# Optimization experiments

Hardware: AMD Instinct MI355X
Metric: run time of the kernel (lower is better)

The kernel has to match this reference:

```python
import jax, jax.numpy as jnp
import numpy as np

D = 1024
H = 16
DK = D // H
HID = 4096
EPS = 1e-5


def setup_inputs() -> dict:
    key = jax.random.key(0)
    ks = jax.random.split(key, 16)
    B, S = 2, 2048
    sc = lambda fan_in: 1.0 / np.sqrt(fan_in)
    inp = {
        "x": jax.random.normal(ks[0], (B, S, D), jnp.float32),
        "y": jax.random.normal(ks[1], (B, S, D), jnp.float32),
        "mask": jnp.ones((B, 1, 1, S), jnp.int32),
        # attention projections, stored [in, out]
        "Wq": jax.random.normal(ks[2], (D, D), jnp.float32) * sc(D),
        "bq": jnp.zeros((D,), jnp.float32),
        "Wk": jax.random.normal(ks[3], (D, D), jnp.float32) * sc(D),
        "bk": jnp.zeros((D,), jnp.float32),
        "Wv": jax.random.normal(ks[4], (D, D), jnp.float32) * sc(D),
        "bv": jnp.zeros((D,), jnp.float32),
        "Wo": jax.random.normal(ks[5], (D, D), jnp.float32) * sc(D),
        "bo": jnp.zeros((D,), jnp.float32),
        # FFN
        "W1": jax.random.normal(ks[6], (D, HID), jnp.float32) * sc(D),
        "b1": jnp.zeros((HID,), jnp.float32),
        "W2": jax.random.normal(ks[7], (HID, D), jnp.float32) * sc(HID),
        "b2": jnp.zeros((D,), jnp.float32),
        # LayerNorms
        "g1": jnp.ones((D,), jnp.float32),
        "be1": jnp.zeros((D,), jnp.float32),
        "g2": jnp.ones((D,), jnp.float32),
        "be2": jnp.zeros((D,), jnp.float32),
    }
    return inp


def _layer_norm(x, g, b):
    m = jnp.mean(x, axis=-1, keepdims=True)
    v = jnp.mean(jnp.square(x - m), axis=-1, keepdims=True)
    return (x - m) * jax.lax.rsqrt(v + EPS) * g + b


def _split_heads(t):  # [B,S,D] -> [B,H,S,DK]
    B, S, _ = t.shape
    return t.reshape(B, S, H, DK).transpose(0, 2, 1, 3)


def reference(x, y, mask, Wq, bq, Wk, bk, Wv, bv, Wo, bo,
              W1, b1, W2, b2, g1, be1, g2, be2):
    scale = 1.0 / np.sqrt(DK)
    Q = _split_heads(x @ Wq + bq)
    K = _split_heads(y @ Wk + bk)
    V = _split_heads(y @ Wv + bv)
    scores = jnp.einsum("bhqd,bhkd->bhqk", Q, K) * scale  # [B,H,S,S]
    scores = jnp.where(mask == 0, jnp.float32(-1e9), scores)
    probs = jax.nn.softmax(scores, axis=-1)
    attn = jnp.einsum("bhqk,bhkd->bhqd", probs, V)
    B, _, S, _ = attn.shape
    attn = attn.transpose(0, 2, 1, 3).reshape(B, S, D)
    mha_out = attn @ Wo + bo
    x1 = _layer_norm(x + mha_out, g1, be1)
    ff = jax.nn.relu(x1 @ W1 + b1) @ W2 + b2
    return _layer_norm(x1 + ff, g2, be2)
```

## Files before the change

### kernel.cpp

```cpp
#include <hip/hip_runtime.h>

#define S_ 2048
#define D_ 1024
#define B_ 2
#define H_ 16
#define DK_ 64
#define HID_ 4096

typedef unsigned short u16;
typedef __attribute__((ext_vector_type(8))) short short8;
typedef __attribute__((ext_vector_type(4))) float f32x4;

#define SLOT(q16, r16) (((q16) * 16) + ((r16) ^ (q16)))

__device__ __forceinline__ float bf2f(u16 u) {
  return __uint_as_float(((unsigned int)u) << 16);
}
__device__ __forceinline__ u16 f2bf(float f) {
  unsigned int x = __float_as_uint(f);
  x += 0x7fff + ((x >> 16) & 1);
  return (u16)(x >> 16);
}
__device__ __forceinline__ unsigned int pk2bf(float lo, float hi) {
  return ((__float_as_uint(lo) + 0x8000u) >> 16) | ((__float_as_uint(hi) + 0x8000u) & 0xffff0000u);
}

__global__ void prep_k(
    const float* __restrict__ Wq, const float* __restrict__ Wk,
    const float* __restrict__ Wv, const float* __restrict__ Wo,
    const float* __restrict__ W1, const float* __restrict__ W2,
    u16* __restrict__ WqT, u16* __restrict__ WkT, u16* __restrict__ WvT,
    u16* __restrict__ WoT, u16* __restrict__ W1T, u16* __restrict__ W2T) {
  const int z = blockIdx.z;
  __shared__ u16 tile[32][33];
  const float* in; u16* outp; int R, C;
  switch (z) {
    case 0: in = Wq; outp = WqT; R = 1024; C = 1024; break;
    case 1: in = Wk; outp = WkT; R = 1024; C = 1024; break;
    case 2: in = Wv; outp = WvT; R = 1024; C = 1024; break;
    case 3: in = Wo; outp = WoT; R = 1024; C = 1024; break;
    case 4: in = W1; outp = W1T; R = 1024; C = 4096; break;
    default: in = W2; outp = W2T; R = 4096; C = 1024; break;
  }
  int c0, r0;
  if (z == 5) { c0 = blockIdx.y * 32; r0 = blockIdx.x * 32; }
  else        { c0 = blockIdx.x * 32; r0 = blockIdx.y * 32; }
  if (c0 >= C || r0 >= R) return;
  const int tx = threadIdx.x, ty = threadIdx.y;
  for (int i = ty; i < 32; i += 8)
    tile[i][tx] = f2bf(in[(long)(r0 + i) * C + c0 + tx]);
  __syncthreads();
  for (int i = ty; i < 32; i += 8)
    outp[(long)(c0 + i) * R + r0 + tx] = tile[tx][i];
}

__global__ __launch_bounds__(256) void cvt2_k(const float* __restrict__ x, const float* __restrict__ y,
                                              u16* __restrict__ xb, u16* __restrict__ yb) {
  const int z = blockIdx.y;
  const float* in = z ? y : x;
  u16* outp = z ? yb : xb;
  const int i = blockIdx.x * 256 + threadIdx.x;
  float4 v = ((const float4*)in)[i];
  unsigned int lo = (unsigned int)f2bf(v.x) | ((unsigned int)f2bf(v.y) << 16);
  unsigned int hi = (unsigned int)f2bf(v.z) | ((unsigned int)f2bf(v.w) << 16);
  ((uint2*)outp)[i] = make_uint2(lo, hi);
}

template<int MT, int NT, int OUTF32>
__global__ __launch_bounds__(256) void gemm_bt(
    const u16* __restrict__ A, const u16* __restrict__ Bt,
    const float* __restrict__ bias, void* __restrict__ Cv,
    int K, int lda, int ldb, int ldc,
    long sA, long sB, long sC, int relu) {
  constexpr int BM = MT * 32;
  constexpr int BN = NT * 32;
  __shared__ __align__(16) u16 As[BM * 32];
  __shared__ __align__(16) u16 Bs[BN * 32];
  const int z = blockIdx.z;
  A  += (long)z * sA;
  Bt += (long)z * sB;
  const int tid  = threadIdx.x;
  const int lane = tid & 63, wave = tid >> 6;
  const int quad = lane >> 4, l15 = lane & 15;
  const int wm = wave >> 1, wn = wave & 1;
  const u16* Ab = A  + (long)(blockIdx.y * BM) * lda;
  const u16* Bb = Bt + (long)(blockIdx.x * BN) * ldb;

  f32x4 acc[MT][NT];
#pragma unroll
  for (int i = 0; i < MT; ++i)
#pragma unroll
    for (int j = 0; j < NT; ++j) acc[i][j] = (f32x4){0.f, 0.f, 0.f, 0.f};

  const int r0  = tid >> 2;
  const int kk0 = (tid & 3) * 8;

  for (int kt = 0; kt < K; kt += 32) {
#pragma unroll
    for (int p = 0; p < BM / 64; ++p) {
      __builtin_amdgcn_global_load_lds(
          (const __attribute__((address_space(1))) void*)(Ab + (long)(p * 64 + r0) * lda + kt + kk0),
          (__attribute__((address_space(3))) void*)(&As[p * 2048 + tid * 8]), 16, 0, 0);
    }
#pragma unroll
    for (int p = 0; p < BN / 64; ++p) {
      __builtin_amdgcn_global_load_lds(
          (const __attribute__((address_space(1))) void*)(Bb + (long)(p * 64 + r0) * ldb + kt + kk0),
          (__attribute__((address_space(3))) void*)(&Bs[p * 2048 + tid * 8]), 16, 0, 0);
    }
    __syncthreads();
    short8 af[MT], bfr[NT];
#pragma unroll
    for (int mt = 0; mt < MT; ++mt)
      af[mt] = *(const short8*)&As[(wm * (MT * 16) + mt * 16 + l15) * 32 + quad * 8];
#pragma unroll
    for (int nt = 0; nt < NT; ++nt)
      bfr[nt] = *(const short8*)&Bs[(wn * (NT * 16) + nt * 16 + l15) * 32 + quad * 8];
#pragma unroll
    for (int mt = 0; mt < MT; ++mt)
#pragma unroll
      for (int nt = 0; nt < NT; ++nt)
        acc[mt][nt] = __builtin_amdgcn_mfma_f32_16x16x32_bf16(af[mt], bfr[nt], acc[mt][nt], 0, 0, 0);
    __syncthreads();
  }

#pragma unroll
  for (int nt = 0; nt < NT; ++nt) {
    const int col = blockIdx.x * BN + wn * (NT * 16) + nt * 16 + l15;
    const float bvv = bias ? bias[col] : 0.f;
#pragma unroll
    for (int mt = 0; mt < MT; ++mt) {
#pragma unroll
      for (int r = 0; r < 4; ++r) {
        const int row = blockIdx.y * BM + wm * (MT * 16) + mt * 16 + quad * 4 + r;
        float v = acc[mt][nt][r] + bvv;
        if (relu) v = fmaxf(v, 0.f);
        if (OUTF32) ((float*)Cv)[(long)z * sC + (long)row * ldc + col] = v;
        else        ((u16*)Cv)[(long)z * sC + (long)row * ldc + col] = f2bf(v);
      }
    }
  }
}

template<int RELU>
__global__ __launch_bounds__(512, 2) void gemm256_k(
    const u16* __restrict__ A, const u16* __restrict__ Bt,
    const float* __restrict__ bias, u16* __restrict__ C,
    int K, int lda, int ldb, int ldc, int kOff, long sC) {
  __shared__ __align__(16) u16 lds[65536];
  const int z = blockIdx.z;
  A  += (long)z * kOff;
  Bt += (long)z * kOff;
  const int tid = threadIdx.x;
  const int lane = tid & 63, w = tid >> 6;
  const int quad = lane >> 4, l15 = lane & 15;
  const int wm = w >> 2, wn = w & 3;
  const int bx = blockIdx.x, by = blockIdx.y;

  const int srow = w * 16 + l15;
  const u16* a0p = A + (long)(by * 256 + srow) * lda + quad * 8;
  const u16* a1p = a0p + (long)128 * lda;
  const u16* b0p = Bt + (long)(bx * 256 + srow) * ldb + quad * 8;
  const u16* b1p = b0p + (long)128 * ldb;

  f32x4 acc[8][4];
#pragma unroll
  for (int i = 0; i < 8; ++i)
#pragma unroll
    for (int j = 0; j < 4; ++j) acc[i][j] = (f32x4){0.f, 0.f, 0.f, 0.f};

  auto STAGE = [&](int c) {
    const int sl = (c & 3) * 8192;
    const long ko = (long)c * 32;
    __builtin_amdgcn_global_load_lds(
        (const __attribute__((address_space(1))) void*)(a0p + ko),
        (__attribute__((address_space(3))) void*)(&lds[sl + tid * 8]), 16, 0, 0);
    __builtin_amdgcn_global_load_lds(
        (const __attribute__((address_space(1))) void*)(a1p + ko),
        (__attribute__((address_space(3))) void*)(&lds[sl + 4096 + tid * 8]), 16, 0, 0);
    __builtin_amdgcn_global_load_lds(
        (const __attribute__((address_space(1))) void*)(b0p + ko),
        (__attribute__((address_space(3))) void*)(&lds[32768 + sl + tid * 8]), 16, 0, 0);
    __builtin_amdgcn_global_load_lds(
        (const __attribute__((address_space(1))) void*)(b1p + ko),
        (__attribute__((address_space(3))) void*)(&lds[32768 + sl + 4096 + tid * 8]), 16, 0, 0);
  };

  auto COMPUTE = [&](int t) {
    const int sl = (t & 3) * 8192;
    short8 af[8], bfv[4];
#pragma unroll
    for (int fr = 0; fr < 8; ++fr)
      af[fr] = *(const short8*)&lds[sl + ((wm * 8 + fr) * 64 + lane) * 8];
#pragma unroll
    for (int fc = 0; fc < 4; ++fc)
      bfv[fc] = *(const short8*)&lds[32768 + sl + ((wn * 4 + fc) * 64 + lane) * 8];
    __builtin_amdgcn_s_setprio(1);
#pragma unroll
    for (int fr = 0; fr < 8; ++fr)
#pragma unroll
      for (int fc = 0; fc < 4; ++fc)
        acc[fr][fc] = __builtin_amdgcn_mfma_f32_16x16x32_bf16(af[fr], bfv[fc], acc[fr][fc], 0, 0, 0);
    __builtin_amdgcn_s_setprio(0);
  };

  const int NT = K >> 5;
  STAGE(0); STAGE(1); STAGE(2);
  for (int t = 0; t < NT - 2; ++t) {
    asm volatile("s_waitcnt vmcnt(8)" ::: "memory");
    __builtin_amdgcn_s_barrier();
    __builtin_amdgcn_sched_barrier(0);
    if (t + 3 < NT) STAGE(t + 3);
    COMPUTE(t);
  }
  asm volatile("s_waitcnt vmcnt(4)" ::: "memory");
  __builtin_amdgcn_s_barrier();
  __builtin_amdgcn_sched_barrier(0);
  COMPUTE(NT - 2);
  asm volatile("s_waitcnt vmcnt(0)" ::: "memory");
  __builtin_amdgcn_s_barrier();
  __builtin_amdgcn_sched_barrier(0);
  COMPUTE(NT - 1);

  C += (long)z * sC;
#pragma unroll
  for (int fc = 0; fc < 4; ++fc) {
    const int col = bx * 256 + wn * 64 + fc * 16 + l15;
    const float bvv = bias ? bias[col] : 0.f;
#pragma unroll
    for (int fr = 0; fr < 8; ++fr) {
      const long row = by * 256 + wm * 128 + fr * 16 + quad * 4;
#pragma unroll
      for (int r = 0; r < 4; ++r) {
        float v = acc[fr][fc][r] + bvv;
        if (RELU) v = fmaxf(v, 0.f);
        C[(row + r) * ldc + col] = f2bf(v);
      }
    }
  }
}

__global__ __launch_bounds__(256) void qkv_k(
    const u16* __restrict__ xb, const u16* __restrict__ yb,
    const u16* __restrict__ WqT, const u16* __restrict__ WkT, const u16* __restrict__ WvT,
    const float* __restrict__ bq, const float* __restrict__ bk, const float* __restrict__ bv,
    u16* __restrict__ Q, u16* __restrict__ Kp, u16* __restrict__ Vp) {
  __shared__ __align__(16) u16 As[128 * 32];
  __shared__ __align__(16) u16 Bs[128 * 32];
  const int z = blockIdx.z;
  const u16* A  = (z == 0) ? xb : yb;
  const u16* Bt = (z == 0) ? WqT : (z == 1) ? WkT : WvT;
  const float* bias = (z == 0) ? bq : (z == 1) ? bk : bv;
  u16* C = (z == 0) ? Q : (z == 1) ? Kp : Vp;
  const float sc = (z == 0) ? 0.18033688011112042f : 1.0f;
  const int tid  = threadIdx.x;
  const int lane = tid & 63, wave = tid >> 6;
  const int quad = lane >> 4, l15 = lane & 15;
  const int wm = wave >> 1, wn = wave & 1;
  const u16* Ab = A  + (long)(blockIdx.y * 128) * D_;
  const u16* Bb = Bt + (long)(blockIdx.x * 128) * D_;

  f32x4 acc[4][4];
#pragma unroll
  for (int i = 0; i < 4; ++i)
#pragma unroll
    for (int j = 0; j < 4; ++j) acc[i][j] = (f32x4){0.f, 0.f, 0.f, 0.f};

  const int r0  = tid >> 2;
  const int kk0 = (tid & 3) * 8;

  for (int kt = 0; kt < D_; kt += 32) {
#pragma unroll
    for (int p = 0; p < 2; ++p) {
      __builtin_amdgcn_global_load_lds(
          (const __attribute__((address_space(1))) void*)(Ab + (long)(p * 64 + r0) * D_ + kt + kk0),
          (__attribute__((address_space(3))) void*)(&As[p * 2048 + tid * 8]), 16, 0, 0);
      __builtin_amdgcn_global_load_lds(
          (const __attribute__((address_space(1))) void*)(Bb + (long)(p * 64 + r0) * D_ + kt + kk0),
          (__attribute__((address_space(3))) void*)(&Bs[p * 2048 + tid * 8]), 16, 0, 0);
    }
    __syncthreads();
    short8 af[4], bfr[4];
#pragma unroll
    for (int mt = 0; mt < 4; ++mt)
      af[mt] = *(const short8*)&As[(wm * 64 + mt * 16 + l15) * 32 + quad * 8];
#pragma unroll
    for (int nt = 0; nt < 4; ++nt)
      bfr[nt] = *(const short8*)&Bs[(wn * 64 + nt * 16 + l15) * 32 + quad * 8];
#pragma unroll
    for (int mt = 0; mt < 4; ++mt)
#pragma unroll
      for (int nt = 0; nt < 4; ++nt)
        acc[mt][nt] = __builtin_amdgcn_mfma_f32_16x16x32_bf16(af[mt], bfr[nt], acc[mt][nt], 0, 0, 0);
    __syncthreads();
  }

#pragma unroll
  for (int nt = 0; nt < 4; ++nt) {
    const int col = blockIdx.x * 128 + wn * 64 + nt * 16 + l15;
    const float bvv = bias[col];
#pragma unroll
    for (int mt = 0; mt < 4; ++mt) {
#pragma unroll
      for (int r = 0; r < 4; ++r) {
        const int row = blockIdx.y * 128 + wm * 64 + mt * 16 + quad * 4 + r;
        C[(long)row * D_ + col] = f2bf((acc[mt][nt][r] + bvv) * sc);
      }
    }
  }
}

__global__ void vtrans_k(const u16* __restrict__ V, u16* __restrict__ Vt) {
  __shared__ u16 tile[32][33];
  const int bh = blockIdx.z, b = bh >> 4, h = bh & 15;
  const u16* in = V + (long)b * S_ * D_ + h * DK_;
  u16* outp = Vt + (long)bh * DK_ * S_;
  const int s0 = blockIdx.x * 32, d0 = blockIdx.y * 32;
  const int tx = threadIdx.x, ty = threadIdx.y;
  for (int i = ty; i < 32; i += 8)
    tile[i][tx] = in[(long)(s0 + i) * D_ + d0 + tx];
  __syncthreads();
  for (int i = ty; i < 32; i += 8)
    outp[(long)(d0 + i) * S_ + s0 + tx] = tile[tx][i];
}

__global__ __launch_bounds__(256, 4) void flash_k(
    const u16* __restrict__ Q, const u16* __restrict__ Kp, const u16* __restrict__ Vt,
    const int* __restrict__ mask, u16* __restrict__ ctx) {
  __shared__ __align__(16) u16 sQ[8192];
  __shared__ __align__(16) u16 sK[2][2048];
  __shared__ __align__(16) u16 sV[2][2048];
  __shared__ __align__(16) u16 sP[4][1024];

  const int bh = blockIdx.x, qt = blockIdx.y;
  const int b = bh >> 4, h = bh & 15;
  const int tid = threadIdx.x;
  const int w = tid >> 6, lane = tid & 63;
  const int quad = lane >> 4, l15 = lane & 15;

  const u16* Qg  = Q  + ((long)b * S_ + qt * 128) * D_ + h * DK_;
  const u16* Kg  = Kp + (long)b * S_ * D_ + h * DK_;
  const u16* Vtg = Vt + (long)bh * DK_ * S_;
  const int* maskg = mask + (long)b * S_;
  u16* ctxg = ctx + ((long)b * S_ + qt * 128) * D_ + h * DK_;

  const int krow = tid >> 3, kc = tid & 7;
  const u16* kptr = Kg + (long)krow * D_ + kc * 8;
  const int ksw = (((krow >> 4) * 2 + (kc >> 2)) * 64 + SLOT(kc & 3, krow & 15)) * 8;
  const int vrow = tid >> 2, vc = tid & 3;
  const u16* vptr = Vtg + (long)vrow * S_ + vc * 8;
  const int vsw = ((vrow >> 4) * 64 + SLOT(vc, vrow & 15)) * 8;

  uint4 kreg = *(const uint4*)kptr;
  uint4 vreg = *(const uint4*)vptr;

#pragma unroll
  for (int p = 0; p < 4; ++p) {
    const int idx = p * 256 + tid;
    const int row = idx >> 3, cb = idx & 7;
    uint4 v = *(const uint4*)(Qg + (long)row * D_ + cb * 8);
    *(uint4*)&sQ[(((row >> 4) * 2 + (cb >> 2)) * 64 + SLOT(cb & 3, row & 15)) * 8] = v;
  }
  *(uint4*)&sK[0][ksw] = kreg;
  *(uint4*)&sV[0][vsw] = vreg;
  kreg = *(const uint4*)(kptr + 32 * D_);
  vreg = *(const uint4*)(vptr + 32);
  kptr += 64 * D_;
  vptr += 64;
  __syncthreads();

  const int rslot = SLOT(quad, l15) * 8;

  short8 qf[2][2];
#pragma unroll
  for (int mf = 0; mf < 2; ++mf)
#pragma unroll
    for (int kt = 0; kt < 2; ++kt)
      qf[mf][kt] = *(const short8*)&sQ[(((w * 2 + mf) * 2 + kt) * 64) * 8 + rslot];

  float lsum[2] = {0.f, 0.f};
  f32x4 accO[2][4];
#pragma unroll
  for (int i = 0; i < 2; ++i)
#pragma unroll
    for (int j = 0; j < 4; ++j) accO[i][j] = (f32x4){0.f, 0.f, 0.f, 0.f};

  for (int t = 0; t < 64; ++t) {
    if (t) __syncthreads();
    const int buf = t & 1, nb = buf ^ 1;
    if (t < 63) {
      *(uint4*)&sK[nb][ksw] = kreg;
      *(uint4*)&sV[nb][vsw] = vreg;
      if (t < 62) {
        kreg = *(const uint4*)kptr;
        vreg = *(const uint4*)vptr;
        kptr += 32 * D_;
        vptr += 32;
      }
    }
    f32x4 accS[2][2];
#pragma unroll
    for (int i = 0; i < 2; ++i)
#pragma unroll
      for (int j = 0; j < 2; ++j) accS[i][j] = (f32x4){0.f, 0.f, 0.f, 0.f};
#pragma unroll
    for (int kt = 0; kt < 2; ++kt) {
      short8 kf0 = *(const short8*)&sK[buf][(kt * 64) * 8 + rslot];
      short8 kf1 = *(const short8*)&sK[buf][((2 + kt) * 64) * 8 + rslot];
#pragma unroll
      for (int mf = 0; mf < 2; ++mf) {
        accS[0][mf] = __builtin_amdgcn_mfma_f32_16x16x32_bf16(kf0, qf[mf][kt], accS[0][mf], 0, 0, 0);
        accS[1][mf] = __builtin_amdgcn_mfma_f32_16x16x32_bf16(kf1, qf[mf][kt], accS[1][mf], 0, 0, 0);
      }
    }
    const int4 mv0 = *(const int4*)(maskg + t * 32 + quad * 4);
    const int4 mv1 = *(const int4*)(maskg + t * 32 + 16 + quad * 4);
#pragma unroll
    for (int mk = 0; mk < 2; ++mk) {
      const int4 mv = mk ? mv1 : mv0;
      const int qt2 = mk * 2 + (quad >> 1);
      const int j0 = (quad & 1) * 4;
#pragma unroll
      for (int mf = 0; mf < 2; ++mf) {
        float p0 = mv.x ? __builtin_amdgcn_exp2f(accS[mk][mf][0]) : 0.f;
        float p1 = mv.y ? __builtin_amdgcn_exp2f(accS[mk][mf][1]) : 0.f;
        float p2 = mv.z ? __builtin_amdgcn_exp2f(accS[mk][mf][2]) : 0.f;
        float p3 = mv.w ? __builtin_amdgcn_exp2f(accS[mk][mf][3]) : 0.f;
        lsum[mf] += (p0 + p1) + (p2 + p3);
        *(uint2*)&sP[w][(mf * 64 + SLOT(qt2, l15)) * 8 + j0] =
            make_uint2(pk2bf(p0, p1), pk2bf(p2, p3));
      }
    }
    short8 pf0 = *(const short8*)&sP[w][0 + rslot];
    short8 pf1 = *(const short8*)&sP[w][64 * 8 + rslot];
#pragma unroll
    for (int n = 0; n < 4; ++n) {
      short8 vf = *(const short8*)&sV[buf][(n * 64) * 8 + rslot];
      accO[0][n] = __builtin_amdgcn_mfma_f32_16x16x32_bf16(pf0, vf, accO[0][n], 0, 0, 0);
      accO[1][n] = __builtin_amdgcn_mfma_f32_16x16x32_bf16(pf1, vf, accO[1][n], 0, 0, 0);
    }
  }

#pragma unroll
  for (int mf = 0; mf < 2; ++mf) {
    lsum[mf] += __shfl_xor(lsum[mf], 16, 64);
    lsum[mf] += __shfl_xor(lsum[mf], 32, 64);
  }
#pragma unroll
  for (int mf = 0; mf < 2; ++mf) {
    float inv[4];
#pragma unroll
    for (int r = 0; r < 4; ++r)
      inv[r] = 1.f / __shfl(lsum[mf], quad * 4 + r, 64);
#pragma unroll
    for (int n = 0; n < 4; ++n) {
#pragma unroll
      for (int r = 0; r < 4; ++r)
        ctxg[(long)(w * 32 + mf * 16 + quad * 4 + r) * D_ + n * 16 + l15] =
            f2bf(accO[mf][n][r] * inv[r]);
    }
  }
}

__device__ __forceinline__ float block_reduce_sum(float v, float* red) {
#pragma unroll
  for (int off = 32; off; off >>= 1) v += __shfl_down(v, off, 64);
  __syncthreads();
  if ((threadIdx.x & 63) == 0) red[threadIdx.x >> 6] = v;
  __syncthreads();
  return red[0] + red[1] + red[2] + red[3];
}

__global__ __launch_bounds__(256) void addln_fb(const float* __restrict__ A,
    const u16* __restrict__ M0, const u16* __restrict__ M1, const float* __restrict__ bo,
    const float* __restrict__ g, const float* __restrict__ be, u16* __restrict__ outp) {
  __shared__ float red[4];
  const int row = blockIdx.x, tid = threadIdx.x;
  const float4 av = ((const float4*)(A + (long)row * D_))[tid];
  const uint2 m0 = ((const uint2*)(M0 + (long)row * D_))[tid];
  const uint2 m1 = ((const uint2*)(M1 + (long)row * D_))[tid];
  const int c0 = tid * 4;
  float xv[4];
  xv[0] = av.x + bf2f((u16)(m0.x & 0xffff)) + bf2f((u16)(m1.x & 0xffff)) + bo[c0 + 0];
  xv[1] = av.y + bf2f((u16)(m0.x >> 16))    + bf2f((u16)(m1.x >> 16))    + bo[c0 + 1];
  xv[2] = av.z + bf2f((u16)(m0.y & 0xffff)) + bf2f((u16)(m1.y & 0xffff)) + bo[c0 + 2];
  xv[3] = av.w + bf2f((u16)(m0.y >> 16))    + bf2f((u16)(m1.y >> 16))    + bo[c0 + 3];
  float s  = xv[0] + xv[1] + xv[2] + xv[3];
  float ss = xv[0]*xv[0] + xv[1]*xv[1] + xv[2]*xv[2] + xv[3]*xv[3];
  s  = block_reduce_sum(s, red);
  ss = block_reduce_sum(ss, red);
  const float m   = s * (1.0f / 1024.0f);
  const float var = ss * (1.0f / 1024.0f) - m * m;
  const float rs  = rsqrtf(var + 1e-5f);
  float v0 = (xv[0] - m) * rs * g[c0 + 0] + be[c0 + 0];
  float v1 = (xv[1] - m) * rs * g[c0 + 1] + be[c0 + 1];
  float v2 = (xv[2] - m) * rs * g[c0 + 2] + be[c0 + 2];
  float v3 = (xv[3] - m) * rs * g[c0 + 3] + be[c0 + 3];
  unsigned int o01 = (unsigned int)f2bf(v0) | ((unsigned int)f2bf(v1) << 16);
  unsigned int o23 = (unsigned int)f2bf(v2) | ((unsigned int)f2bf(v3) << 16);
  ((uint2*)(outp + (long)row * D_))[tid] = make_uint2(o01, o23);
}

__global__ __launch_bounds__(256) void addln2_bf(const u16* __restrict__ A,
    const u16* __restrict__ F0, const u16* __restrict__ F1,
    const u16* __restrict__ F2, const u16* __restrict__ F3,
    const float* __restrict__ b2,
    const float* __restrict__ g, const float* __restrict__ be, float* __restrict__ outp) {
  __shared__ float red[4];
  const int row = blockIdx.x, tid = threadIdx.x;
  const uint2 av = ((const uint2*)(A + (long)row * D_))[tid];
  const uint2 f0 = ((const uint2*)(F0 + (long)row * D_))[tid];
  const uint2 f1 = ((const uint2*)(F1 + (long)row * D_))[tid];
  const uint2 f2 = ((const uint2*)(F2 + (long)row * D_))[tid];
  const uint2 f3 = ((const uint2*)(F3 + (long)row * D_))[tid];
  const int c0 = tid * 4;
  float xv[4];
  xv[0] = bf2f((u16)(av.x & 0xffff)) + bf2f((u16)(f0.x & 0xffff)) + bf2f((u16)(f1.x & 0xffff))
        + bf2f((u16)(f2.x & 0xffff)) + bf2f((u16)(f3.x & 0xffff)) + b2[c0 + 0];
  xv[1] = bf2f((u16)(av.x >> 16))    + bf2f((u16)(f0.x >> 16))    + bf2f((u16)(f1.x >> 16))
        + bf2f((u16)(f2.x >> 16))    + bf2f((u16)(f3.x >> 16))    + b2[c0 + 1];
  xv[2] = bf2f((u16)(av.y & 0xffff)) + bf2f((u16)(f0.y & 0xffff)) + bf2f((u16)(f1.y & 0xffff))
        + bf2f((u16)(f2.y & 0xffff)) + bf2f((u16)(f3.y & 0xffff)) + b2[c0 + 2];
  xv[3] = bf2f((u16)(av.y >> 16))    + bf2f((u16)(f0.y >> 16))    + bf2f((u16)(f1.y >> 16))
        + bf2f((u16)(f2.y >> 16))    + bf2f((u16)(f3.y >> 16))    + b2[c0 + 3];
  float s  = xv[0] + xv[1] + xv[2] + xv[3];
  float ss = xv[0]*xv[0] + xv[1]*xv[1] + xv[2]*xv[2] + xv[3]*xv[3];
  s  = block_reduce_sum(s, red);
  ss = block_reduce_sum(ss, red);
  const float m   = s * (1.0f / 1024.0f);
  const float var = ss * (1.0f / 1024.0f) - m * m;
  const float rs  = rsqrtf(var + 1e-5f);
  float4 o;
  o.x = (xv[0] - m) * rs * g[c0 + 0] + be[c0 + 0];
  o.y = (xv[1] - m) * rs * g[c0 + 1] + be[c0 + 1];
  o.z = (xv[2] - m) * rs * g[c0 + 2] + be[c0 + 2];
  o.w = (xv[3] - m) * rs * g[c0 + 3] + be[c0 + 3];
  ((float4*)(outp + (long)row * D_))[tid] = o;
}

extern "C" void kernel_launch(void* const* d_in, const int* in_sizes, int n_in,
                              void* d_out, int out_size, void* d_ws, size_t ws_size,
                              hipStream_t stream) {
  const float* x   = (const float*)d_in[0];
  const float* y   = (const float*)d_in[1];
  const int* mask  = (const int*)d_in[2];
  const float* Wq = (const float*)d_in[3];  const float* bq = (const float*)d_in[4];
  const float* Wk = (const float*)d_in[5];  const float* bk = (const float*)d_in[6];
  const float* Wv = (const float*)d_in[7];  const float* bv = (const float*)d_in[8];
  const float* Wo = (const float*)d_in[9];  const float* bo = (const float*)d_in[10];
  const float* W1 = (const float*)d_in[11]; const float* b1 = (const float*)d_in[12];
  const float* W2 = (const float*)d_in[13]; const float* b2 = (const float*)d_in[14];
  const float* g1 = (const float*)d_in[15]; const float* be1 = (const float*)d_in[16];
  const float* g2 = (const float*)d_in[17]; const float* be2 = (const float*)d_in[18];
  float* out = (float*)d_out;

  char* w = (char*)d_ws;
  const size_t MB = 1024 * 1024;
  u16* WqT = (u16*)(w + 0 * MB);
  u16* WkT = (u16*)(w + 2 * MB);
  u16* WvT = (u16*)(w + 4 * MB);
  u16* WoT = (u16*)(w + 6 * MB);
  u16* W1T = (u16*)(w + 8 * MB);
  u16* W2T = (u16*)(w + 16 * MB);
  u16* xb  = (u16*)(w + 24 * MB);
  u16* yb  = (u16*)(w + 32 * MB);
  u16* Q   = (u16*)(w + 40 * MB);
  u16* Kp  = (u16*)(w + 48 * MB);
  u16* Vp  = (u16*)(w + 56 * MB);
  u16* Vt  = (u16*)(w + 64 * MB);
  u16* ctx = (u16*)(w + 72 * MB);
  u16* mha = (u16*)(w + 80 * MB);
  u16* x1  = (u16*)(w + 24 * MB);
  u16* h1  = (u16*)(w + 96 * MB);
  u16* ff  = (u16*)(w + 40 * MB);

  prep_k<<<dim3(128, 32, 6), dim3(32, 8), 0, stream>>>(Wq, Wk, Wv, Wo, W1, W2,
      WqT, WkT, WvT, WoT, W1T, W2T);
  cvt2_k<<<dim3(4096, 2), 256, 0, stream>>>(x, y, xb, yb);

  qkv_k<<<dim3(8, 32, 3), 256, 0, stream>>>(xb, yb, WqT, WkT, WvT, bq, bk, bv, Q, Kp, Vp);

  vtrans_k<<<dim3(64, 2, 32), dim3(32, 8), 0, stream>>>(Vp, Vt);

  flash_k<<<dim3(32, 16), 256, 0, stream>>>(Q, Kp, Vt, mask, ctx);

  gemm_bt<4, 4, 0><<<dim3(8, 32, 2), 256, 0, stream>>>(ctx, WoT, nullptr, mha,
      512, 1024, 1024, 1024, 512, 512, (long)4096 * 1024, 0);
  addln_fb<<<dim3(4096), 256, 0, stream>>>(x, mha, mha + (long)4096 * 1024, bo, g1, be1, x1);

  gemm256_k<1><<<dim3(16, 16, 1), 512, 0, stream>>>(x1, W1T, b1, h1,
      1024, 1024, 1024, 4096, 0, 0);
  gemm256_k<0><<<dim3(4, 16, 4), 512, 0, stream>>>(h1, W2T, nullptr, ff,
      1024, 4096, 4096, 1024, 1024, (long)4096 * 1024);
  addln2_bf<<<dim3(4096), 256, 0, stream>>>(x1, ff, ff + (long)4096 * 1024,
      ff + (long)2 * 4096 * 1024, ff + (long)3 * 4096 * 1024, b2, g2, be2, out);
}
```

Measured before the change: 393.3 us.

## Use pipelined 256-tile GEMMs for QKV and Wo, register-resident P in attention

```diff
diff --git a/kernel.cpp b/kernel.cpp
--- a/kernel.cpp
+++ b/kernel.cpp
@@ -9,6 +9,7 @@
 
 typedef unsigned short u16;
 typedef __attribute__((ext_vector_type(8))) short short8;
+typedef __attribute__((ext_vector_type(4))) short s16x4;
 typedef __attribute__((ext_vector_type(4))) float f32x4;
 
 #define SLOT(q16, r16) (((q16) * 16) + ((r16) ^ (q16)))
@@ -23,6 +24,14 @@
 }
 __device__ __forceinline__ unsigned int pk2bf(float lo, float hi) {
   return ((__float_as_uint(lo) + 0x8000u) >> 16) | ((__float_as_uint(hi) + 0x8000u) & 0xffff0000u);
+}
+
+__device__ __forceinline__ f32x4 mfma16(s16x4 a, s16x4 b, f32x4 c) {
+#if __has_builtin(__builtin_amdgcn_mfma_f32_16x16x16_bf16)
+  return __builtin_amdgcn_mfma_f32_16x16x16_bf16(a, b, c, 0, 0, 0);
+#else
+  return __builtin_amdgcn_mfma_f32_16x16x16bf16_1k(a, b, c, 0, 0, 0);
+#endif
 }
 
 __global__ void prep_k(
@@ -66,82 +75,6 @@
   ((uint2*)outp)[i] = make_uint2(lo, hi);
 }
 
-template<int MT, int NT, int OUTF32>
-__global__ __launch_bounds__(256) void gemm_bt(
-    const u16* __restrict__ A, const u16* __restrict__ Bt,
-    const float* __restrict__ bias, void* __restrict__ Cv,
-    int K, int lda, int ldb, int ldc,
-    long sA, long sB, long sC, int relu) {
-  constexpr int BM = MT * 32;
-  constexpr int BN = NT * 32;
-  __shared__ __align__(16) u16 As[BM * 32];
-  __shared__ __align__(16) u16 Bs[BN * 32];
-  const int z = blockIdx.z;
-  A  += (long)z * sA;
-  Bt += (long)z * sB;
-  const int tid  = threadIdx.x;
-  const int lane = tid & 63, wave = tid >> 6;
-  const int quad = lane >> 4, l15 = lane & 15;
-  const int wm = wave >> 1, wn = wave & 1;
-  const u16* Ab = A  + (long)(blockIdx.y * BM) * lda;
-  const u16* Bb = Bt + (long)(blockIdx.x * BN) * ldb;
-
-  f32x4 acc[MT][NT];
-#pragma unroll
-  for (int i = 0; i < MT; ++i)
-#pragma unroll
-    for (int j = 0; j < NT; ++j) acc[i][j] = (f32x4){0.f, 0.f, 0.f, 0.f};
-
-  const int r0  = tid >> 2;
-  const int kk0 = (tid & 3) * 8;
-
-  for (int kt = 0; kt < K; kt += 32) {
-#pragma unroll
-    for (int p = 0; p < BM / 64; ++p) {
-      __builtin_amdgcn_global_load_lds(
-          (const __attribute__((address_space(1))) void*)(Ab + (long)(p * 64 + r0) * lda + kt + kk0),
-          (__attribute__((address_space(3))) void*)(&As[p * 2048 + tid * 8]), 16, 0, 0);
-    }
-#pragma unroll
-    for (int p = 0; p < BN / 64; ++p) {
-      __builtin_amdgcn_global_load_lds(
-          (const __attribute__((address_space(1))) void*)(Bb + (long)(p * 64 + r0) * ldb + kt + kk0),
-          (__attribute__((address_space(3))) void*)(&Bs[p * 2048 + tid * 8]), 16, 0, 0);
-    }
-    __syncthreads();
-    short8 af[MT], bfr[NT];
-#pragma unroll
-    for (int mt = 0; mt < MT; ++mt)
-      af[mt] = *(const short8*)&As[(wm * (MT * 16) + mt * 16 + l15) * 32 + quad * 8];
-#pragma unroll
-    for (int nt = 0; nt < NT; ++nt)
-      bfr[nt] = *(const short8*)&Bs[(wn * (NT * 16) + nt * 16 + l15) * 32 + quad * 8];
-#pragma unroll
-    for (int mt = 0; mt < MT; ++mt)
-#pragma unroll
-      for (int nt = 0; nt < NT; ++nt)
-        acc[mt][nt] = __builtin_amdgcn_mfma_f32_16x16x32_bf16(af[mt], bfr[nt], acc[mt][nt], 0, 0, 0);
-    __syncthreads();
-  }
-
-#pragma unroll
-  for (int nt = 0; nt < NT; ++nt) {
-    const int col = blockIdx.x * BN + wn * (NT * 16) + nt * 16 + l15;
-    const float bvv = bias ? bias[col] : 0.f;
-#pragma unroll
-    for (int mt = 0; mt < MT; ++mt) {
-#pragma unroll
-      for (int r = 0; r < 4; ++r) {
-        const int row = blockIdx.y * BM + wm * (MT * 16) + mt * 16 + quad * 4 + r;
-        float v = acc[mt][nt][r] + bvv;
-        if (relu) v = fmaxf(v, 0.f);
-        if (OUTF32) ((float*)Cv)[(long)z * sC + (long)row * ldc + col] = v;
-        else        ((u16*)Cv)[(long)z * sC + (long)row * ldc + col] = f2bf(v);
-      }
-    }
-  }
-}
-
 template<int RELU>
 __global__ __launch_bounds__(512, 2) void gemm256_k(
     const u16* __restrict__ A, const u16* __restrict__ Bt,
@@ -240,72 +173,99 @@
   }
 }
 
-__global__ __launch_bounds__(256) void qkv_k(
+__global__ __launch_bounds__(512, 2) void qkv256_k(
     const u16* __restrict__ xb, const u16* __restrict__ yb,
     const u16* __restrict__ WqT, const u16* __restrict__ WkT, const u16* __restrict__ WvT,
     const float* __restrict__ bq, const float* __restrict__ bk, const float* __restrict__ bv,
-    u16* __restrict__ Q, u16* __restrict__ Kp, u16* __restrict__ Vp) {
-  __shared__ __align__(16) u16 As[128 * 32];
-  __shared__ __align__(16) u16 Bs[128 * 32];
+    u16* __restrict__ Qo, u16* __restrict__ Ko, u16* __restrict__ Vo) {
+  __shared__ __align__(16) u16 lds[65536];
   const int z = blockIdx.z;
   const u16* A  = (z == 0) ? xb : yb;
   const u16* Bt = (z == 0) ? WqT : (z == 1) ? WkT : WvT;
   const float* bias = (z == 0) ? bq : (z == 1) ? bk : bv;
-  u16* C = (z == 0) ? Q : (z == 1) ? Kp : Vp;
+  u16* C = (z == 0) ? Qo : (z == 1) ? Ko : Vo;
   const float sc = (z == 0) ? 0.18033688011112042f : 1.0f;
-  const int tid  = threadIdx.x;
-  const int lane = tid & 63, wave = tid >> 6;
+  const int tid = threadIdx.x;
+  const int lane = tid & 63, w = tid >> 6;
   const int quad = lane >> 4, l15 = lane & 15;
-  const int wm = wave >> 1, wn = wave & 1;
-  const u16* Ab = A  + (long)(blockIdx.y * 128) * D_;
-  const u16* Bb = Bt + (long)(blockIdx.x * 128) * D_;
-
-  f32x4 acc[4][4];
-#pragma unroll
-  for (int i = 0; i < 4; ++i)
+  const int wm = w >> 2, wn = w & 3;
+  const int bx = blockIdx.x, by = blockIdx.y;
+
+  const int srow = w * 16 + l15;
+  const u16* a0p = A + (long)(by * 256 + srow) * D_ + quad * 8;
+  const u16* a1p = a0p + (long)128 * D_;
+  const u16* b0p = Bt + (long)(bx * 256 + srow) * D_ + quad * 8;
+  const u16* b1p = b0p + (long)128 * D_;
+
+  f32x4 acc[8][4];
+#pragma unroll
+  for (int i = 0; i < 8; ++i)
 #pragma unroll
     for (int j = 0; j < 4; ++j) acc[i][j] = (f32x4){0.f, 0.f, 0.f, 0.f};
 
-  const int r0  = tid >> 2;
-  const int kk0 = (tid & 3) * 8;
-
-  for (int kt = 0; kt < D_; kt += 32) {
-#pragma unroll
-    for (int p = 0; p < 2; ++p) {
-      __builtin_amdgcn_global_load_lds(
-          (const __attribute__((address_space(1))) void*)(Ab + (long)(p * 64 + r0) * D_ + kt + kk0),
-          (__attribute__((address_space(3))) void*)(&As[p * 2048 + tid * 8]), 16, 0, 0);
-      __builtin_amdgcn_global_load_lds(
-          (const __attribute__((address_space(1))) void*)(Bb + (long)(p * 64 + r0) * D_ + kt + kk0),
-          (__attribute__((address_space(3))) void*)(&Bs[p * 2048 + tid * 8]), 16, 0, 0);
-    }
-    __syncthreads();
-    short8 af[4], bfr[4];
-#pragma unroll
-    for (int mt = 0; mt < 4; ++mt)
-      af[mt] = *(const short8*)&As[(wm * 64 + mt * 16 + l15) * 32 + quad * 8];
-#pragma unroll
-    for (int nt = 0; nt < 4; ++nt)
-      bfr[nt] = *(const short8*)&Bs[(wn * 64 + nt * 16 + l15) * 32 + quad * 8];
-#pragma unroll
-    for (int mt = 0; mt < 4; ++mt)
-#pragma unroll
-      for (int nt = 0; nt < 4; ++nt)
-        acc[mt][nt] = __builtin_amdgcn_mfma_f32_16x16x32_bf16(af[mt], bfr[nt], acc[mt][nt], 0, 0, 0);
-    __syncthreads();
-  }
-
-#pragma unroll
-  for (int nt = 0; nt < 4; ++nt) {
-    const int col = blockIdx.x * 128 + wn * 64 + nt * 16 + l15;
+  auto STAGE = [&](int c) {
+    const int sl = (c & 3) * 8192;
+    const long ko = (long)c * 32;
+    __builtin_amdgcn_global_load_lds(
+        (const __attribute__((address_space(1))) void*)(a0p + ko),
+        (__attribute__((address_space(3))) void*)(&lds[sl + tid * 8]), 16, 0, 0);
+    __builtin_amdgcn_global_load_lds(
+        (const __attribute__((address_space(1))) void*)(a1p + ko),
+        (__attribute__((address_space(3))) void*)(&lds[sl + 4096 + tid * 8]), 16, 0, 0);
+    __builtin_amdgcn_global_load_lds(
+        (const __attribute__((address_space(1))) void*)(b0p + ko),
+        (__attribute__((address_space(3))) void*)(&lds[32768 + sl + tid * 8]), 16, 0, 0);
+    __builtin_amdgcn_global_load_lds(
+        (const __attribute__((address_space(1))) void*)(b1p + ko),
+        (__attribute__((address_space(3))) void*)(&lds[32768 + sl + 4096 + tid * 8]), 16, 0, 0);
+  };
+
+  auto COMPUTE = [&](int t) {
+    const int sl = (t & 3) * 8192;
+    short8 af[8], bfv[4];
+#pragma unroll
+    for (int fr = 0; fr < 8; ++fr)
+      af[fr] = *(const short8*)&lds[sl + ((wm * 8 + fr) * 64 + lane) * 8];
+#pragma unroll
+    for (int fc = 0; fc < 4; ++fc)
+      bfv[fc] = *(const short8*)&lds[32768 + sl + ((wn * 4 + fc) * 64 + lane) * 8];
+    __builtin_amdgcn_s_setprio(1);
+#pragma unroll
+    for (int fr = 0; fr < 8; ++fr)
+#pragma unroll
+      for (int fc = 0; fc < 4; ++fc)
+        acc[fr][fc] = __builtin_amdgcn_mfma_f32_16x16x32_bf16(af[fr], bfv[fc], acc[fr][fc], 0, 0, 0);
+    __builtin_amdgcn_s_setprio(0);
+  };
+
+  const int NT = D_ >> 5;
+  STAGE(0); STAGE(1); STAGE(2);
+  for (int t = 0; t < NT - 2; ++t) {
+    asm volatile("s_waitcnt vmcnt(8)" ::: "memory");
+    __builtin_amdgcn_s_barrier();
+    __builtin_amdgcn_sched_barrier(0);
+    if (t + 3 < NT) STAGE(t + 3);
+    COMPUTE(t);
+  }
+  asm volatile("s_waitcnt vmcnt(4)" ::: "memory");
+  __builtin_amdgcn_s_barrier();
+  __builtin_amdgcn_sched_barrier(0);
+  COMPUTE(NT - 2);
+  asm volatile("s_waitcnt vmcnt(0)" ::: "memory");
+  __builtin_amdgcn_s_barrier();
+  __builtin_amdgcn_sched_barrier(0);
+  COMPUTE(NT - 1);
+
+#pragma unroll
+  for (int fc = 0; fc < 4; ++fc) {
+    const int col = bx * 256 + wn * 64 + fc * 16 + l15;
     const float bvv = bias[col];
 #pragma unroll
-    for (int mt = 0; mt < 4; ++mt) {
-#pragma unroll
-      for (int r = 0; r < 4; ++r) {
-        const int row = blockIdx.y * 128 + wm * 64 + mt * 16 + quad * 4 + r;
-        C[(long)row * D_ + col] = f2bf((acc[mt][nt][r] + bvv) * sc);
-      }
+    for (int fr = 0; fr < 8; ++fr) {
+      const long row = by * 256 + wm * 128 + fr * 16 + quad * 4;
+#pragma unroll
+      for (int r = 0; r < 4; ++r)
+        C[(row + r) * D_ + col] = f2bf((acc[fr][fc][r] + bvv) * sc);
     }
   }
 }
@@ -330,7 +290,7 @@
   __shared__ __align__(16) u16 sQ[8192];
   __shared__ __align__(16) u16 sK[2][2048];
   __shared__ __align__(16) u16 sV[2][2048];
-  __shared__ __align__(16) u16 sP[4][1024];
+  __shared__ int s_allones;
 
   const int bh = blockIdx.x, qt = blockIdx.y;
   const int b = bh >> 4, h = bh & 15;
@@ -347,12 +307,17 @@
   const int krow = tid >> 3, kc = tid & 7;
   const u16* kptr = Kg + (long)krow * D_ + kc * 8;
   const int ksw = (((krow >> 4) * 2 + (kc >> 2)) * 64 + SLOT(kc & 3, krow & 15)) * 8;
-  const int vrow = tid >> 2, vc = tid & 3;
-  const u16* vptr = Vtg + (long)vrow * S_ + vc * 8;
-  const int vsw = ((vrow >> 4) * 64 + SLOT(vc, vrow & 15)) * 8;
+  const int vd  = ((tid >> 6) << 4) | (tid & 15);
+  const int vq4 = ((tid >> 4) & 3) * 4;
+  const u16* vptr = Vtg + (long)vd * S_ + vq4;
 
   uint4 kreg = *(const uint4*)kptr;
-  uint4 vreg = *(const uint4*)vptr;
+  uint2 vlo = *(const uint2*)vptr;
+  uint2 vhi = *(const uint2*)(vptr + 16);
+
+  int part = 1;
+  for (int i = tid; i < S_; i += 256) part &= (maskg[i] != 0);
+  if (tid == 0) s_allones = 1;
 
 #pragma unroll
   for (int p = 0; p < 4; ++p) {
@@ -362,9 +327,10 @@
     *(uint4*)&sQ[(((row >> 4) * 2 + (cb >> 2)) * 64 + SLOT(cb & 3, row & 15)) * 8] = v;
   }
   *(uint4*)&sK[0][ksw] = kreg;
-  *(uint4*)&sV[0][vsw] = vreg;
+  *(uint4*)&sV[0][tid * 8] = make_uint4(vlo.x, vlo.y, vhi.x, vhi.y);
   kreg = *(const uint4*)(kptr + 32 * D_);
-  vreg = *(const uint4*)(vptr + 32);
+  vlo = *(const uint2*)(vptr + 32);
+  vhi = *(const uint2*)(vptr + 48);
   kptr += 64 * D_;
   vptr += 64;
   __syncthreads();
@@ -378,22 +344,27 @@
     for (int kt = 0; kt < 2; ++kt)
       qf[mf][kt] = *(const short8*)&sQ[(((w * 2 + mf) * 2 + kt) * 64) * 8 + rslot];
 
+  if (!part) s_allones = 0;
+  __syncthreads();
+  const int allones = s_allones;
+
   float lsum[2] = {0.f, 0.f};
-  f32x4 accO[2][4];
+  f32x4 accOT[2][4];
 #pragma unroll
   for (int i = 0; i < 2; ++i)
 #pragma unroll
-    for (int j = 0; j < 4; ++j) accO[i][j] = (f32x4){0.f, 0.f, 0.f, 0.f};
+    for (int j = 0; j < 4; ++j) accOT[i][j] = (f32x4){0.f, 0.f, 0.f, 0.f};
 
   for (int t = 0; t < 64; ++t) {
     if (t) __syncthreads();
     const int buf = t & 1, nb = buf ^ 1;
     if (t < 63) {
       *(uint4*)&sK[nb][ksw] = kreg;
-      *(uint4*)&sV[nb][vsw] = vreg;
+      *(uint4*)&sV[nb][tid * 8] = make_uint4(vlo.x, vlo.y, vhi.x, vhi.y);
       if (t < 62) {
         kreg = *(const uint4*)kptr;
-        vreg = *(const uint4*)vptr;
+        vlo = *(const uint2*)vptr;
+        vhi = *(const uint2*)(vptr + 16);
         kptr += 32 * D_;
         vptr += 32;
       }
@@ -413,31 +384,46 @@
         accS[1][mf] = __builtin_amdgcn_mfma_f32_16x16x32_bf16(kf1, qf[mf][kt], accS[1][mf], 0, 0, 0);
       }
     }
-    const int4 mv0 = *(const int4*)(maskg + t * 32 + quad * 4);
-    const int4 mv1 = *(const int4*)(maskg + t * 32 + 16 + quad * 4);
-#pragma unroll
-    for (int mk = 0; mk < 2; ++mk) {
-      const int4 mv = mk ? mv1 : mv0;
-      const int qt2 = mk * 2 + (quad >> 1);
-      const int j0 = (quad & 1) * 4;
+    s16x4 pb[2][2];
+    if (allones) {
+#pragma unroll
+      for (int mk = 0; mk < 2; ++mk)
+#pragma unroll
+        for (int mf = 0; mf < 2; ++mf) {
+          float p0 = __builtin_amdgcn_exp2f(accS[mk][mf][0]);
+          float p1 = __builtin_amdgcn_exp2f(accS[mk][mf][1]);
+          float p2 = __builtin_amdgcn_exp2f(accS[mk][mf][2]);
+          float p3 = __builtin_amdgcn_exp2f(accS[mk][mf][3]);
+          lsum[mf] += (p0 + p1) + (p2 + p3);
+          *(uint2*)&pb[mk][mf] = make_uint2(pk2bf(p0, p1), pk2bf(p2, p3));
+        }
+    } else {
+      const int4 mv0 = *(const int4*)(maskg + t * 32 + quad * 4);
+      const int4 mv1 = *(const int4*)(maskg + t * 32 + 16 + quad * 4);
+#pragma unroll
+      for (int mk = 0; mk < 2; ++mk) {
+        const int4 mv = mk ? mv1 : mv0;
+#pragma unroll
+        for (int mf = 0; mf < 2; ++mf) {
+          float p0 = mv.x ? __builtin_amdgcn_exp2f(accS[mk][mf][0]) : 0.f;
+          float p1 = mv.y ? __builtin_amdgcn_exp2f(accS[mk][mf][1]) : 0.f;
+          float p2 = mv.z ? __builtin_amdgcn_exp2f(accS[mk][mf][2]) : 0.f;
+          float p3 = mv.w ? __builtin_amdgcn_exp2f(accS[mk][mf][3]) : 0.f;
+          lsum[mf] += (p0 + p1) + (p2 + p3);
+          *(uint2*)&pb[mk][mf] = make_uint2(pk2bf(p0, p1), pk2bf(p2, p3));
+        }
+      }
+    }
+#pragma unroll
+    for (int n = 0; n < 4; ++n) {
+      short8 vv = *(const short8*)&sV[buf][(n * 64 + lane) * 8];
+      s16x4 v0 = __builtin_shufflevector(vv, vv, 0, 1, 2, 3);
+      s16x4 v1 = __builtin_shufflevector(vv, vv, 4, 5, 6, 7);
 #pragma unroll
       for (int mf = 0; mf < 2; ++mf) {
-        float p0 = mv.x ? __builtin_amdgcn_exp2f(accS[mk][mf][0]) : 0.f;
-        float p1 = mv.y ? __builtin_amdgcn_exp2f(accS[mk][mf][1]) : 0.f;
-        float p2 = mv.z ? __builtin_amdgcn_exp2f(accS[mk][mf][2]) : 0.f;
-        float p3 = mv.w ? __builtin_amdgcn_exp2f(accS[mk][mf][3]) : 0.f;
-        lsum[mf] += (p0 + p1) + (p2 + p3);
-        *(uint2*)&sP[w][(mf * 64 + SLOT(qt2, l15)) * 8 + j0] =
-            make_uint2(pk2bf(p0, p1), pk2bf(p2, p3));
+        accOT[mf][n] = mfma16(v0, pb[0][mf], accOT[mf][n]);
+        accOT[mf][n] = mfma16(v1, pb[1][mf], accOT[mf][n]);
       }
-    }
-    short8 pf0 = *(const short8*)&sP[w][0 + rslot];
-    short8 pf1 = *(const short8*)&sP[w][64 * 8 + rslot];
-#pragma unroll
-    for (int n = 0; n < 4; ++n) {
-      short8 vf = *(const short8*)&sV[buf][(n * 64) * 8 + rslot];
-      accO[0][n] = __builtin_amdgcn_mfma_f32_16x16x32_bf16(pf0, vf, accO[0][n], 0, 0, 0);
-      accO[1][n] = __builtin_amdgcn_mfma_f32_16x16x32_bf16(pf1, vf, accO[1][n], 0, 0, 0);
     }
   }
 
@@ -446,18 +432,18 @@
     lsum[mf] += __shfl_xor(lsum[mf], 16, 64);
     lsum[mf] += __shfl_xor(lsum[mf], 32, 64);
   }
+  const float inv0 = 1.f / lsum[0], inv1 = 1.f / lsum[1];
 #pragma unroll
   for (int mf = 0; mf < 2; ++mf) {
-    float inv[4];
-#pragma unroll
-    for (int r = 0; r < 4; ++r)
-      inv[r] = 1.f / __shfl(lsum[mf], quad * 4 + r, 64);
+    const float iv = mf ? inv1 : inv0;
+    u16* cp = ctxg + (long)(w * 32 + mf * 16 + l15) * D_;
 #pragma unroll
     for (int n = 0; n < 4; ++n) {
-#pragma unroll
-      for (int r = 0; r < 4; ++r)
-        ctxg[(long)(w * 32 + mf * 16 + quad * 4 + r) * D_ + n * 16 + l15] =
-            f2bf(accO[mf][n][r] * inv[r]);
+      float o0 = accOT[mf][n][0] * iv;
+      float o1 = accOT[mf][n][1] * iv;
+      float o2 = accOT[mf][n][2] * iv;
+      float o3 = accOT[mf][n][3] * iv;
+      *(uint2*)(cp + n * 16 + quad * 4) = make_uint2(pk2bf(o0, o1), pk2bf(o2, o3));
     }
   }
 }
@@ -472,19 +458,27 @@
 }
 
 __global__ __launch_bounds__(256) void addln_fb(const float* __restrict__ A,
-    const u16* __restrict__ M0, const u16* __restrict__ M1, const float* __restrict__ bo,
+    const u16* __restrict__ M0, const u16* __restrict__ M1,
+    const u16* __restrict__ M2, const u16* __restrict__ M3,
+    const float* __restrict__ bo,
     const float* __restrict__ g, const float* __restrict__ be, u16* __restrict__ outp) {
   __shared__ float red[4];
   const int row = blockIdx.x, tid = threadIdx.x;
   const float4 av = ((const float4*)(A + (long)row * D_))[tid];
   const uint2 m0 = ((const uint2*)(M0 + (long)row * D_))[tid];
   const uint2 m1 = ((const uint2*)(M1 + (long)row * D_))[tid];
+  const uint2 m2 = ((const uint2*)(M2 + (long)row * D_))[tid];
+  const uint2 m3 = ((const uint2*)(M3 + (long)row * D_))[tid];
   const int c0 = tid * 4;
   float xv[4];
-  xv[0] = av.x + bf2f((u16)(m0.x & 0xffff)) + bf2f((u16)(m1.x & 0xffff)) + bo[c0 + 0];
-  xv[1] = av.y + bf2f((u16)(m0.x >> 16))    + bf2f((u16)(m1.x >> 16))    + bo[c0 + 1];
-  xv[2] = av.z + bf2f((u16)(m0.y & 0xffff)) + bf2f((u16)(m1.y & 0xffff)) + bo[c0 + 2];
-  xv[3] = av.w + bf2f((u16)(m0.y >> 16))    + bf2f((u16)(m1.y >> 16))    + bo[c0 + 3];
+  xv[0] = av.x + bf2f((u16)(m0.x & 0xffff)) + bf2f((u16)(m1.x & 0xffff))
+               + bf2f((u16)(m2.x & 0xffff)) + bf2f((u16)(m3.x & 0xffff)) + bo[c0 + 0];
+  xv[1] = av.y + bf2f((u16)(m0.x >> 16))    + bf2f((u16)(m1.x >> 16))
+               + bf2f((u16)(m2.x >> 16))    + bf2f((u16)(m3.x >> 16))    + bo[c0 + 1];
+  xv[2] = av.z + bf2f((u16)(m0.y & 0xffff)) + bf2f((u16)(m1.y & 0xffff))
+               + bf2f((u16)(m2.y & 0xffff)) + bf2f((u16)(m3.y & 0xffff)) + bo[c0 + 2];
+  xv[3] = av.w + bf2f((u16)(m0.y >> 16))    + bf2f((u16)(m1.y >> 16))
+               + bf2f((u16)(m2.y >> 16))    + bf2f((u16)(m3.y >> 16))    + bo[c0 + 3];
   float s  = xv[0] + xv[1] + xv[2] + xv[3];
   float ss = xv[0]*xv[0] + xv[1]*xv[1] + xv[2]*xv[2] + xv[3]*xv[3];
   s  = block_reduce_sum(s, red);
@@ -578,15 +572,16 @@
       WqT, WkT, WvT, WoT, W1T, W2T);
   cvt2_k<<<dim3(4096, 2), 256, 0, stream>>>(x, y, xb, yb);
 
-  qkv_k<<<dim3(8, 32, 3), 256, 0, stream>>>(xb, yb, WqT, WkT, WvT, bq, bk, bv, Q, Kp, Vp);
+  qkv256_k<<<dim3(4, 16, 3), 512, 0, stream>>>(xb, yb, WqT, WkT, WvT, bq, bk, bv, Q, Kp, Vp);
 
   vtrans_k<<<dim3(64, 2, 32), dim3(32, 8), 0, stream>>>(Vp, Vt);
 
   flash_k<<<dim3(32, 16), 256, 0, stream>>>(Q, Kp, Vt, mask, ctx);
 
-  gemm_bt<4, 4, 0><<<dim3(8, 32, 2), 256, 0, stream>>>(ctx, WoT, nullptr, mha,
-      512, 1024, 1024, 1024, 512, 512, (long)4096 * 1024, 0);
-  addln_fb<<<dim3(4096), 256, 0, stream>>>(x, mha, mha + (long)4096 * 1024, bo, g1, be1, x1);
+  gemm256_k<0><<<dim3(4, 16, 4), 512, 0, stream>>>(ctx, WoT, nullptr, mha,
+      256, 1024, 1024, 1024, 256, (long)4096 * 1024);
+  addln_fb<<<dim3(4096), 256, 0, stream>>>(x, mha, mha + (long)4096 * 1024,
+      mha + (long)2 * 4096 * 1024, mha + (long)3 * 4096 * 1024, bo, g1, be1, x1);
 
   gemm256_k<1><<<dim3(16, 16, 1), 512, 0, stream>>>(x1, W1T, b1, h1,
       1024, 1024, 1024, 4096, 0, 0);
```

Result: slower. 412.4 us (+4.9%).
